# Kernel optimization log

Measured on AMD Instinct MI355X. Metric: run time of the kernel, lower is better.

The kernel has to match this reference:

```python
import jax, jax.numpy as jnp
import numpy as np

N = 4194304          # flat pixel batch (~2 full 1080p frames)
NUM_CAMERAS = 8
NUM_FRAMES = 1000
EPS = 1e-6


def setup_inputs() -> dict:
    key = jax.random.key(0)
    ks = jax.random.split(key, 8)
    W, H = 1920, 1080
    exposure_params = 0.2 * jax.random.normal(ks[0], (NUM_FRAMES,), jnp.float32)
    vignetting_params = 0.05 * jax.random.normal(ks[1], (NUM_CAMERAS, 3, 5), jnp.float32)
    color_params = 0.05 * jax.random.normal(ks[2], (NUM_FRAMES, 8), jnp.float32)
    # CRF raw init matching the module: softplus-inverse of 1.0 with minima (0.3,0.3,0.1), offset 0
    def _sp_inv(x, m):
        return float(np.log(np.expm1(max(1e-5, x - m))))
    crf0 = jnp.array([_sp_inv(1.0, 0.3), _sp_inv(1.0, 0.3), _sp_inv(1.0, 0.1), 0.0], jnp.float32)
    crf_params = (jnp.broadcast_to(crf0, (NUM_CAMERAS, 3, 4))
                  + 0.05 * jax.random.normal(ks[3], (NUM_CAMERAS, 3, 4), jnp.float32))
    rgb = jax.random.uniform(ks[4], (N, 3), jnp.float32)
    pixel_coords = jax.random.uniform(ks[5], (N, 2), jnp.float32) * jnp.array([W, H], jnp.float32)
    camera_idcs = jax.random.randint(ks[6], (N,), 0, NUM_CAMERAS, jnp.int32)
    frame_idcs = jax.random.randint(ks[7], (N,), 0, NUM_FRAMES, jnp.int32)
    return dict(exposure_params=exposure_params, vignetting_params=vignetting_params,
                color_params=color_params, crf_params=crf_params, rgb=rgb,
                pixel_coords=pixel_coords, camera_idcs=camera_idcs, frame_idcs=frame_idcs,
                resolution_w=W, resolution_h=H)


def _ppisp(exposure_params, vignetting_params, color_params, crf_params,
           rgb, pixel_coords, camera_idcs, frame_idcs, resolution_w, resolution_h):
    # 1) per-frame exposure (EV scale)
    exp_scale = jnp.exp2(exposure_params[frame_idcs])[:, None]            # [N,1]
    x = rgb * exp_scale                                                    # [N,3]

    # 2) per-camera, per-channel radial vignetting: params = [cx, cy, a1, a2, a3]
    vig = vignetting_params[camera_idcs]                                   # [N,3,5]
    u = pixel_coords[:, 0] / jnp.float32(resolution_w) - 0.5               # [N]
    v = pixel_coords[:, 1] / jnp.float32(resolution_h) - 0.5               # [N]
    du = u[:, None] - vig[..., 0]                                          # [N,3]
    dv = v[:, None] - vig[..., 1]
    r2 = du * du + dv * dv                                                 # [N,3]
    falloff = 1.0 + r2 * (vig[..., 2] + r2 * (vig[..., 3] + r2 * vig[..., 4]))
    x = x * falloff

    # 3) per-frame color: WB gains (r,b) + off-diagonal 3x3 mixing matrix (8 params)
    cp = color_params[frame_idcs]                                          # [N,8]
    gains = jnp.stack([jnp.exp(cp[:, 0]), jnp.ones_like(cp[:, 0]), jnp.exp(cp[:, 1])], axis=-1)
    x = x * gains
    one = jnp.ones_like(cp[:, 0])
    M = jnp.stack([
        jnp.stack([one,      cp[:, 2], cp[:, 3]], axis=-1),
        jnp.stack([cp[:, 4], one,      cp[:, 5]], axis=-1),
        jnp.stack([cp[:, 6], cp[:, 7], one     ], axis=-1)], axis=-2)      # [N,3,3]
    x = jnp.einsum('nij,nj->ni', M, x)

    # 4) per-camera, per-channel 4-param sigmoid CRF, identity at init
    crf = crf_params[camera_idcs]                                          # [N,3,4]
    a = jax.nn.softplus(crf[..., 0]) + 0.3
    b = jax.nn.softplus(crf[..., 1]) + 0.3
    c = jax.nn.softplus(crf[..., 2]) + 0.1
    d = crf[..., 3]
    xc = jnp.clip(x, EPS, 1.0)
    xa = xc ** a
    out = xa / (xa + (c * (1.0 - xc) + EPS) ** b) + d                      # [N,3]
    return out


def reference(exposure_params, vignetting_params, color_params, crf_params,
              rgb, pixel_coords, camera_idcs, frame_idcs, resolution_w, resolution_h):
    return _ppisp(exposure_params, vignetting_params, color_params, crf_params,
                  rgb, pixel_coords, camera_idcs, frame_idcs, resolution_w, resolution_h)
```

## Files before the change

kernel.cpp:

```cpp
#include <hip/hip_runtime.h>


__global__ void ppisp_precompute(const float* __restrict__ expo,
                                 const float* __restrict__ colorp,
                                 const float* __restrict__ vigp,
                                 const float* __restrict__ crfp,
                                 float* __restrict__ ftab,
                                 float* __restrict__ camtab,
                                 int num_frames) {
    int tid = blockIdx.x * blockDim.x + threadIdx.x;
    if (tid < num_frames) {
        float e = exp2f(expo[tid]);
        const float* cp = colorp + tid * 8;
        float* f = ftab + tid * 12;
        f[0]  = e * expf(cp[0]);
        f[1]  = e;
        f[2]  = e * expf(cp[1]);
        f[3]  = cp[2];
        f[4]  = cp[3];
        f[5]  = cp[4];
        f[6]  = cp[5];
        f[7]  = cp[6];
        f[8]  = cp[7];
        f[9]  = 0.f; f[10] = 0.f; f[11] = 0.f;
    }
    if (tid < 24) {
        const float* vp = vigp + tid * 5;
        const float* cf = crfp + tid * 4;
        float* r = camtab + tid * 12;
        r[0] = vp[0];
        r[1] = vp[1];
        r[2] = vp[2];
        r[3] = vp[3];
        r[4] = vp[4];
        r[5] = log1pf(expf(cf[0])) + 0.3f;
        r[6] = log1pf(expf(cf[1])) + 0.3f;
        r[7] = log1pf(expf(cf[2])) + 0.1f;
        r[8] = cf[3];
        r[9] = 0.f; r[10] = 0.f; r[11] = 0.f;
    }
}

__global__ __launch_bounds__(256) void ppisp_main(
    const float4* __restrict__ rgb4,
    const float4* __restrict__ pc4,
    const int4*   __restrict__ cam4,
    const int4*   __restrict__ frm4,
    const float*  __restrict__ ftab,
    const float*  __restrict__ camtab,
    const int*    __restrict__ resw,
    const int*    __restrict__ resh,
    float4* __restrict__ out4,
    int ngroups) {
    int g = blockIdx.x * blockDim.x + threadIdx.x;
    if (g >= ngroups) return;

    float invW = 1.0f / (float)resw[0];
    float invH = 1.0f / (float)resh[0];

    float4 r0 = rgb4[(size_t)g * 3 + 0];
    float4 r1 = rgb4[(size_t)g * 3 + 1];
    float4 r2v = rgb4[(size_t)g * 3 + 2];
    float4 p0 = pc4[(size_t)g * 2 + 0];
    float4 p1 = pc4[(size_t)g * 2 + 1];
    int4 cams = cam4[g];
    int4 frms = frm4[g];

    float rgb[4][3] = {{r0.x, r0.y, r0.z},
                       {r0.w, r1.x, r1.y},
                       {r1.z, r1.w, r2v.x},
                       {r2v.y, r2v.z, r2v.w}};
    float px[4] = {p0.x, p0.z, p1.x, p1.z};
    float py[4] = {p0.y, p0.w, p1.y, p1.w};
    int camA[4] = {cams.x, cams.y, cams.z, cams.w};
    int frmA[4] = {frms.x, frms.y, frms.z, frms.w};

    float o[12];

#pragma unroll
    for (int p = 0; p < 4; ++p) {
        const float4* fr = (const float4*)(ftab + frmA[p] * 12);
        float4 f0 = fr[0];
        float4 f1 = fr[1];
        float m21 = ((const float*)fr)[8];
        float g3[3] = {f0.x, f0.y, f0.z};

        float u = px[p] * invW - 0.5f;
        float v = py[p] * invH - 0.5f;

        float x[3], av[3], bv[3], cv[3], dv2[3];
#pragma unroll
        for (int ch = 0; ch < 3; ++ch) {
            const float4* cr = (const float4*)(camtab + (camA[p] * 3 + ch) * 12);
            float4 c0 = cr[0];
            float4 c1 = cr[1];
            float dd = ((const float*)cr)[8];
            float du = u - c0.x;
            float dv = v - c0.y;
            float r2 = du * du + dv * dv;
            float fall = 1.0f + r2 * (c0.z + r2 * (c0.w + r2 * c1.x));
            x[ch] = rgb[p][ch] * g3[ch] * fall;
            av[ch] = c1.y; bv[ch] = c1.z; cv[ch] = c1.w; dv2[ch] = dd;
        }

        float y0 = x[0] + f0.w * x[1] + f1.x * x[2];
        float y1 = f1.y * x[0] + x[1] + f1.z * x[2];
        float y2 = f1.w * x[0] + m21 * x[1] + x[2];
        float yv[3] = {y0, y1, y2};

#pragma unroll
        for (int ch = 0; ch < 3; ++ch) {
            float xc = fminf(fmaxf(yv[ch], 1e-6f), 1.0f);
            float la = __builtin_amdgcn_logf(xc);
            float xa = __builtin_amdgcn_exp2f(av[ch] * la);
            float t  = cv[ch] * (1.0f - xc) + 1e-6f;
            float tb = __builtin_amdgcn_exp2f(bv[ch] * __builtin_amdgcn_logf(t));
            o[p * 3 + ch] = xa * __builtin_amdgcn_rcpf(xa + tb) + dv2[ch];
        }
    }

    out4[(size_t)g * 3 + 0] = make_float4(o[0], o[1], o[2], o[3]);
    out4[(size_t)g * 3 + 1] = make_float4(o[4], o[5], o[6], o[7]);
    out4[(size_t)g * 3 + 2] = make_float4(o[8], o[9], o[10], o[11]);
}

extern "C" void kernel_launch(void* const* d_in, const int* in_sizes, int n_in,
                              void* d_out, int out_size, void* d_ws, size_t ws_size,
                              hipStream_t stream) {
    const float* expo   = (const float*)d_in[0];
    const float* vigp   = (const float*)d_in[1];
    const float* colorp = (const float*)d_in[2];
    const float* crfp   = (const float*)d_in[3];
    const float* rgb    = (const float*)d_in[4];
    const float* pc     = (const float*)d_in[5];
    const int*   cam    = (const int*)d_in[6];
    const int*   frm    = (const int*)d_in[7];
    const int*   rw     = (const int*)d_in[8];
    const int*   rh     = (const int*)d_in[9];

    int num_frames = in_sizes[0];
    int N = in_sizes[4] / 3;

    float* ftab = (float*)d_ws;
    size_t ftab_bytes = ((size_t)num_frames * 12 * sizeof(float) + 255) & ~(size_t)255;
    float* camtab = (float*)((char*)d_ws + ftab_bytes);

    int pre_threads = 256;
    int pre_blocks = (num_frames + pre_threads - 1) / pre_threads;
    if (pre_blocks < 1) pre_blocks = 1;
    ppisp_precompute<<<pre_blocks, pre_threads, 0, stream>>>(
        expo, colorp, vigp, crfp, ftab, camtab, num_frames);

    int ngroups = N / 4;
    int threads = 256;
    int blocks = (ngroups + threads - 1) / threads;
    ppisp_main<<<blocks, threads, 0, stream>>>(
        (const float4*)rgb, (const float4*)pc, (const int4*)cam, (const int4*)frm,
        ftab, camtab, rw, rh, (float4*)d_out, ngroups);
}
```

Measured before the change: 214.7 us.

## Stage frame and camera tables in LDS with persistent grid-stride blocks

Repacks the per-frame and per-camera parameter tables from 12 to 10 floats and copies both into shared memory at block start. The main kernel now runs a fixed grid of 2048 blocks, each looping over a contiguous chunk of groups, so the table load is amortised. Random gathers thereby hit LDS instead of global/L2 memory. The costs are about 40KB of shared memory per block, which limits occupancy, a fixed 5000-entry LDS array that assumes at most 1000 frames, and a per-block staging prologue.

```diff
diff --git a/kernel.cpp b/kernel.cpp
--- a/kernel.cpp
+++ b/kernel.cpp
@@ -1,5 +1,8 @@
 #include <hip/hip_runtime.h>
 
+
+#define FREC 5
+#define CREC 5
 
 __global__ void ppisp_precompute(const float* __restrict__ expo,
                                  const float* __restrict__ colorp,
@@ -12,22 +15,22 @@
     if (tid < num_frames) {
         float e = exp2f(expo[tid]);
         const float* cp = colorp + tid * 8;
-        float* f = ftab + tid * 12;
-        f[0]  = e * expf(cp[0]);
-        f[1]  = e;
-        f[2]  = e * expf(cp[1]);
-        f[3]  = cp[2];
-        f[4]  = cp[3];
-        f[5]  = cp[4];
-        f[6]  = cp[5];
-        f[7]  = cp[6];
-        f[8]  = cp[7];
-        f[9]  = 0.f; f[10] = 0.f; f[11] = 0.f;
+        float* f = ftab + tid * 10;
+        f[0] = e * expf(cp[0]);
+        f[1] = e;
+        f[2] = e * expf(cp[1]);
+        f[3] = cp[2];
+        f[4] = cp[3];
+        f[5] = cp[4];
+        f[6] = cp[5];
+        f[7] = cp[6];
+        f[8] = cp[7];
+        f[9] = 0.f;
     }
     if (tid < 24) {
         const float* vp = vigp + tid * 5;
         const float* cf = crfp + tid * 4;
-        float* r = camtab + tid * 12;
+        float* r = camtab + tid * 10;
         r[0] = vp[0];
         r[1] = vp[1];
         r[2] = vp[2];
@@ -37,7 +40,7 @@
         r[6] = log1pf(expf(cf[1])) + 0.3f;
         r[7] = log1pf(expf(cf[2])) + 0.1f;
         r[8] = cf[3];
-        r[9] = 0.f; r[10] = 0.f; r[11] = 0.f;
+        r[9] = 0.f;
     }
 }
 
@@ -46,82 +49,98 @@
     const float4* __restrict__ pc4,
     const int4*   __restrict__ cam4,
     const int4*   __restrict__ frm4,
-    const float*  __restrict__ ftab,
-    const float*  __restrict__ camtab,
+    const float2* __restrict__ ftab2,
+    const float2* __restrict__ camtab2,
     const int*    __restrict__ resw,
     const int*    __restrict__ resh,
     float4* __restrict__ out4,
-    int ngroups) {
-    int g = blockIdx.x * blockDim.x + threadIdx.x;
-    if (g >= ngroups) return;
+    int ngroups, int groups_per_block, int num_frames) {
+    __shared__ float2 sft[5000];
+    __shared__ float2 scam[120];
+
+    int tid = threadIdx.x;
+    int nf2 = num_frames * FREC;
+    for (int i = tid; i < nf2; i += 256) sft[i] = ftab2[i];
+    if (tid < 120) scam[tid] = camtab2[tid];
+    __syncthreads();
 
     float invW = 1.0f / (float)resw[0];
     float invH = 1.0f / (float)resh[0];
 
-    float4 r0 = rgb4[(size_t)g * 3 + 0];
-    float4 r1 = rgb4[(size_t)g * 3 + 1];
-    float4 r2v = rgb4[(size_t)g * 3 + 2];
-    float4 p0 = pc4[(size_t)g * 2 + 0];
-    float4 p1 = pc4[(size_t)g * 2 + 1];
-    int4 cams = cam4[g];
-    int4 frms = frm4[g];
+    int gbase = blockIdx.x * groups_per_block;
+    int gend = gbase + groups_per_block;
+    if (gend > ngroups) gend = ngroups;
 
-    float rgb[4][3] = {{r0.x, r0.y, r0.z},
-                       {r0.w, r1.x, r1.y},
-                       {r1.z, r1.w, r2v.x},
-                       {r2v.y, r2v.z, r2v.w}};
-    float px[4] = {p0.x, p0.z, p1.x, p1.z};
-    float py[4] = {p0.y, p0.w, p1.y, p1.w};
-    int camA[4] = {cams.x, cams.y, cams.z, cams.w};
-    int frmA[4] = {frms.x, frms.y, frms.z, frms.w};
+    for (int g = gbase + tid; g < gend; g += 256) {
+        float4 r0  = rgb4[(size_t)g * 3 + 0];
+        float4 r1  = rgb4[(size_t)g * 3 + 1];
+        float4 r2v = rgb4[(size_t)g * 3 + 2];
+        float4 p0  = pc4[(size_t)g * 2 + 0];
+        float4 p1  = pc4[(size_t)g * 2 + 1];
+        int4 cams = cam4[g];
+        int4 frms = frm4[g];
 
-    float o[12];
+        float rgb[4][3] = {{r0.x, r0.y, r0.z},
+                           {r0.w, r1.x, r1.y},
+                           {r1.z, r1.w, r2v.x},
+                           {r2v.y, r2v.z, r2v.w}};
+        float px[4] = {p0.x, p0.z, p1.x, p1.z};
+        float py[4] = {p0.y, p0.w, p1.y, p1.w};
+        int camA[4] = {cams.x, cams.y, cams.z, cams.w};
+        int frmA[4] = {frms.x, frms.y, frms.z, frms.w};
+
+        float o[12];
 
 #pragma unroll
-    for (int p = 0; p < 4; ++p) {
-        const float4* fr = (const float4*)(ftab + frmA[p] * 12);
-        float4 f0 = fr[0];
-        float4 f1 = fr[1];
-        float m21 = ((const float*)fr)[8];
-        float g3[3] = {f0.x, f0.y, f0.z};
+        for (int p = 0; p < 4; ++p) {
+            int fb = frmA[p] * FREC;
+            float2 F0 = sft[fb + 0];
+            float2 F1 = sft[fb + 1];
+            float2 F2 = sft[fb + 2];
+            float2 F3 = sft[fb + 3];
+            float2 F4 = sft[fb + 4];
+            float g3[3] = {F0.x, F0.y, F1.x};
 
-        float u = px[p] * invW - 0.5f;
-        float v = py[p] * invH - 0.5f;
+            float u = px[p] * invW - 0.5f;
+            float v = py[p] * invH - 0.5f;
 
-        float x[3], av[3], bv[3], cv[3], dv2[3];
+            float x[3], av[3], bv[3], cv[3], dv2[3];
 #pragma unroll
-        for (int ch = 0; ch < 3; ++ch) {
-            const float4* cr = (const float4*)(camtab + (camA[p] * 3 + ch) * 12);
-            float4 c0 = cr[0];
-            float4 c1 = cr[1];
-            float dd = ((const float*)cr)[8];
-            float du = u - c0.x;
-            float dv = v - c0.y;
-            float r2 = du * du + dv * dv;
-            float fall = 1.0f + r2 * (c0.z + r2 * (c0.w + r2 * c1.x));
-            x[ch] = rgb[p][ch] * g3[ch] * fall;
-            av[ch] = c1.y; bv[ch] = c1.z; cv[ch] = c1.w; dv2[ch] = dd;
+            for (int ch = 0; ch < 3; ++ch) {
+                int cb = (camA[p] * 3 + ch) * CREC;
+                float2 C0 = scam[cb + 0];
+                float2 C1 = scam[cb + 1];
+                float2 C2 = scam[cb + 2];
+                float2 C3 = scam[cb + 3];
+                float2 C4 = scam[cb + 4];
+                float du = u - C0.x;
+                float dv = v - C0.y;
+                float r2 = du * du + dv * dv;
+                float fall = 1.0f + r2 * (C1.x + r2 * (C1.y + r2 * C2.x));
+                x[ch] = rgb[p][ch] * g3[ch] * fall;
+                av[ch] = C2.y; bv[ch] = C3.x; cv[ch] = C3.y; dv2[ch] = C4.x;
+            }
+
+            float y0 = x[0] + F1.y * x[1] + F2.x * x[2];
+            float y1 = F2.y * x[0] + x[1] + F3.x * x[2];
+            float y2 = F3.y * x[0] + F4.x * x[1] + x[2];
+            float yv[3] = {y0, y1, y2};
+
+#pragma unroll
+            for (int ch = 0; ch < 3; ++ch) {
+                float xc = fminf(fmaxf(yv[ch], 1e-6f), 1.0f);
+                float la = __builtin_amdgcn_logf(xc);
+                float xa = __builtin_amdgcn_exp2f(av[ch] * la);
+                float t  = cv[ch] * (1.0f - xc) + 1e-6f;
+                float tb = __builtin_amdgcn_exp2f(bv[ch] * __builtin_amdgcn_logf(t));
+                o[p * 3 + ch] = xa * __builtin_amdgcn_rcpf(xa + tb) + dv2[ch];
+            }
         }
 
-        float y0 = x[0] + f0.w * x[1] + f1.x * x[2];
-        float y1 = f1.y * x[0] + x[1] + f1.z * x[2];
-        float y2 = f1.w * x[0] + m21 * x[1] + x[2];
-        float yv[3] = {y0, y1, y2};
-
-#pragma unroll
-        for (int ch = 0; ch < 3; ++ch) {
-            float xc = fminf(fmaxf(yv[ch], 1e-6f), 1.0f);
-            float la = __builtin_amdgcn_logf(xc);
-            float xa = __builtin_amdgcn_exp2f(av[ch] * la);
-            float t  = cv[ch] * (1.0f - xc) + 1e-6f;
-            float tb = __builtin_amdgcn_exp2f(bv[ch] * __builtin_amdgcn_logf(t));
-            o[p * 3 + ch] = xa * __builtin_amdgcn_rcpf(xa + tb) + dv2[ch];
-        }
+        out4[(size_t)g * 3 + 0] = make_float4(o[0], o[1], o[2], o[3]);
+        out4[(size_t)g * 3 + 1] = make_float4(o[4], o[5], o[6], o[7]);
+        out4[(size_t)g * 3 + 2] = make_float4(o[8], o[9], o[10], o[11]);
     }
-
-    out4[(size_t)g * 3 + 0] = make_float4(o[0], o[1], o[2], o[3]);
-    out4[(size_t)g * 3 + 1] = make_float4(o[4], o[5], o[6], o[7]);
-    out4[(size_t)g * 3 + 2] = make_float4(o[8], o[9], o[10], o[11]);
 }
 
 extern "C" void kernel_launch(void* const* d_in, const int* in_sizes, int n_in,
@@ -142,7 +161,7 @@
     int N = in_sizes[4] / 3;
 
     float* ftab = (float*)d_ws;
-    size_t ftab_bytes = ((size_t)num_frames * 12 * sizeof(float) + 255) & ~(size_t)255;
+    size_t ftab_bytes = ((size_t)num_frames * 10 * sizeof(float) + 255) & ~(size_t)255;
     float* camtab = (float*)((char*)d_ws + ftab_bytes);
 
     int pre_threads = 256;
@@ -152,9 +171,10 @@
         expo, colorp, vigp, crfp, ftab, camtab, num_frames);
 
     int ngroups = N / 4;
-    int threads = 256;
-    int blocks = (ngroups + threads - 1) / threads;
-    ppisp_main<<<blocks, threads, 0, stream>>>(
+    int blocks = 2048;
+    int groups_per_block = (ngroups + blocks - 1) / blocks;
+    ppisp_main<<<blocks, 256, 0, stream>>>(
         (const float4*)rgb, (const float4*)pc, (const int4*)cam, (const int4*)frm,
-        ftab, camtab, rw, rh, (float4*)d_out, ngroups);
+        (const float2*)ftab, (const float2*)camtab, rw, rh, (float4*)d_out,
+        ngroups, groups_per_block, num_frames);
 }
```

Result: faster. 186.1 us (-13.3%).
